# Performance work log

Hardware: AMD Instinct MI355X
Metric: run time of the kernel (lower is better)

## Reference

```python
import jax, jax.numpy as jnp
import numpy as np

T = 3          # hparams['T'] message-passing iterations
E = 100000     # num edges (rows of link_state)
M = 200000     # num message pairs
D = 128        # hidden dim of link_state / GRU units
H = 256        # Message MLP hidden width
G = 64         # num graphs


def setup_inputs() -> dict:
    key = jax.random.key(0)
    ks = jax.random.split(key, 16)
    s = 0.05
    inp = {
        'link_state': jax.random.normal(ks[0], (E, D), jnp.float32),
        'states_first': jax.random.randint(ks[1], (M,), 0, E),
        'states_second': jax.random.randint(ks[2], (M,), 0, E),
        'states_graph_ids': jnp.sort(jax.random.randint(ks[3], (E,), 0, G)),
        'sates_num_edges': E,
        # Message MLP: Dense(H, relu) -> Dense(D, relu)
        'mW1': jax.random.normal(ks[4], (2 * D, H), jnp.float32) * s,
        'mb1': jnp.zeros((H,), jnp.float32),
        'mW2': jax.random.normal(ks[5], (H, D), jnp.float32) * s,
        'mb2': jnp.zeros((D,), jnp.float32),
        # GRUCell (keras, reset_after=True): kernel [D,3D], recurrent [D,3D], bias [2,3D]
        'gru_kernel': jax.random.normal(ks[6], (D, 3 * D), jnp.float32) * s,
        'gru_recurrent': jax.random.normal(ks[7], (D, 3 * D), jnp.float32) * s,
        'gru_bias': jnp.zeros((2, 3 * D), jnp.float32),
        # Readout MLP: Dense(H, relu) -> Dense(H, relu) -> Dense(1)
        'rW1': jax.random.normal(ks[8], (D, H), jnp.float32) * s,
        'rb1': jnp.zeros((H,), jnp.float32),
        'rW2': jax.random.normal(ks[9], (H, H), jnp.float32) * s,
        'rb2': jnp.zeros((H,), jnp.float32),
        'rW3': jax.random.normal(ks[10], (H, 1), jnp.float32) * s,
        'rb3': jnp.zeros((1,), jnp.float32),
    }
    return inp


def _gru_step(x, h, kernel, recurrent, bias):
    # keras GRUCell with reset_after=True; gate order: z, r, h
    mx = x @ kernel + bias[0]          # [N, 3D]
    mh = h @ recurrent + bias[1]       # [N, 3D]
    xz, xr, xh = jnp.split(mx, 3, axis=-1)
    hz, hr, hh = jnp.split(mh, 3, axis=-1)
    z = jax.nn.sigmoid(xz + hz)
    r = jax.nn.sigmoid(xr + hr)
    hcand = jnp.tanh(xh + r * hh)
    return z * h + (1.0 - z) * hcand


def reference(link_state, states_first, states_second, states_graph_ids,
              sates_num_edges, mW1, mb1, mW2, mb2,
              gru_kernel, gru_recurrent, gru_bias,
              rW1, rb1, rW2, rb2, rW3, rb3):
    for _ in range(T):
        main_e = link_state[states_first]        # [M, D] gather
        neigh_e = link_state[states_second]      # [M, D] gather
        concat = jnp.concatenate([main_e, neigh_e], axis=1)  # [M, 2D]
        msg = jax.nn.relu(concat @ mW1 + mb1)
        msg = jax.nn.relu(msg @ mW2 + mb2)       # [M, D]
        edges_inputs = jax.ops.segment_sum(msg, states_second,
                                           num_segments=sates_num_edges)  # [E, D]
        link_state = _gru_step(edges_inputs, link_state,
                               gru_kernel, gru_recurrent, gru_bias)
    graph_state = jax.ops.segment_sum(link_state, states_graph_ids,
                                      num_segments=G)  # [G, D]
    r = jax.nn.relu(graph_state @ rW1 + rb1)
    r = jax.nn.relu(r @ rW2 + rb2)
    return r @ rW3 + rb3  # [G, 1]
```

## Files before the change

### kernel.cpp

```cpp
#include <hip/hip_runtime.h>

#define NUM_E 100000
#define NUM_M 200000
#define DIM   128
#define HID   256
#define NG    64
#define TITER 3
#define NB_SCAN 98
#define GS_ER 128

typedef __attribute__((ext_vector_type(8))) short bf16x8;
typedef __attribute__((ext_vector_type(4))) float f32x4;

__device__ __forceinline__ unsigned short f2bf(float f) {
  unsigned u = __float_as_uint(f);
  u += 0x7FFF + ((u >> 16) & 1);
  return (unsigned short)(u >> 16);
}
__device__ __forceinline__ float bf2f(unsigned short h) {
  return __uint_as_float(((unsigned)h) << 16);
}
__device__ __forceinline__ float sigmoidf_(float v) {
  return 1.f / (1.f + __expf(-v));
}
__device__ __forceinline__ float tanhf_(float u) {
  u = fminf(fmaxf(u, -15.f), 15.f);
  float ex = __expf(-2.f * u);
  return (1.f - ex) / (1.f + ex);
}
__device__ __forceinline__ float relu_(float v) { return fmaxf(v, 0.f); }

#define MFMA(a, b, c) __builtin_amdgcn_mfma_f32_16x16x32_bf16((a), (b), (c), 0, 0, 0)

__global__ void hist_kernel(const int* __restrict__ second, int* __restrict__ counts,
                            float4* __restrict__ gs4) {
  int m = blockIdx.x * blockDim.x + threadIdx.x;
  if (m < NG * DIM / 4) gs4[m] = make_float4(0.f, 0.f, 0.f, 0.f);
  if (m < NUM_M) atomicAdd(&counts[second[m]], 1);
}

__global__ __launch_bounds__(256) void scan1_kernel(const int* __restrict__ counts,
                                                    int* __restrict__ partials) {
  __shared__ int sh[256];
  int b = blockIdx.x, t = threadIdx.x;
  int i0 = b * 1024 + t * 4;
  int c0 = (i0 + 0 < NUM_E) ? counts[i0 + 0] : 0;
  int c1 = (i0 + 1 < NUM_E) ? counts[i0 + 1] : 0;
  int c2 = (i0 + 2 < NUM_E) ? counts[i0 + 2] : 0;
  int c3 = (i0 + 3 < NUM_E) ? counts[i0 + 3] : 0;
  int tsum = c0 + c1 + c2 + c3;
  sh[t] = tsum;
  __syncthreads();
  for (int off = 1; off < 256; off <<= 1) {
    int v = (t >= off) ? sh[t - off] : 0;
    __syncthreads();
    sh[t] += v;
    __syncthreads();
  }
  if (t == 255) partials[b] = sh[255];
}

__global__ void scan2_kernel(const int* __restrict__ partials, int* __restrict__ base,
                             int* __restrict__ rowptr) {
  if (threadIdx.x == 0) {
    int run = 0;
    for (int b = 0; b < NB_SCAN; ++b) { base[b] = run; run += partials[b]; }
    rowptr[NUM_E] = NUM_M;
  }
}

__global__ __launch_bounds__(256) void scan3_kernel(const int* __restrict__ counts,
                                                    const int* __restrict__ base,
                                                    int* __restrict__ rowptr) {
  __shared__ int sh[256];
  int b = blockIdx.x, t = threadIdx.x;
  int i0 = b * 1024 + t * 4;
  int c0 = (i0 + 0 < NUM_E) ? counts[i0 + 0] : 0;
  int c1 = (i0 + 1 < NUM_E) ? counts[i0 + 1] : 0;
  int c2 = (i0 + 2 < NUM_E) ? counts[i0 + 2] : 0;
  int c3 = (i0 + 3 < NUM_E) ? counts[i0 + 3] : 0;
  int tsum = c0 + c1 + c2 + c3;
  sh[t] = tsum;
  __syncthreads();
  for (int off = 1; off < 256; off <<= 1) {
    int v = (t >= off) ? sh[t - off] : 0;
    __syncthreads();
    sh[t] += v;
    __syncthreads();
  }
  int p = base[b] + (sh[t] - tsum);
  if (i0 + 0 < NUM_E) rowptr[i0 + 0] = p;
  if (i0 + 1 < NUM_E) rowptr[i0 + 1] = p + c0;
  if (i0 + 2 < NUM_E) rowptr[i0 + 2] = p + c0 + c1;
  if (i0 + 3 < NUM_E) rowptr[i0 + 3] = p + c0 + c1 + c2;
}

__global__ void scatter_kernel(const int* __restrict__ second,
                               const int* __restrict__ rowptr,
                               int* __restrict__ cursor, int* __restrict__ order) {
  int m = blockIdx.x * blockDim.x + threadIdx.x;
  if (m < NUM_M) {
    int e = second[m];
    int pos = atomicAdd(&cursor[e], 1);
    int idx = rowptr[e] + pos;
    if (idx < rowptr[e + 1]) order[idx] = m;
  }
}

__device__ __forceinline__ void pack_range(
    const float* __restrict__ srcA, const float* __restrict__ srcB, int KrowsA,
    int N, int src_ld, int col_off, unsigned short* __restrict__ dst, int idx) {
  int l = idx & 63;
  int t = idx >> 6;
  int NF = N / 16;
  int nf = t % NF;
  int ks = t / NF;
  int n = nf * 16 + (l & 15) + col_off;
  int k0 = ks * 32 + (l >> 4) * 8;
  unsigned short o[8];
  #pragma unroll
  for (int j = 0; j < 8; ++j) {
    int k = k0 + j;
    const float* src = (k < KrowsA) ? (srcA + (size_t)k * src_ld)
                                    : (srcB + (size_t)(k - KrowsA) * src_ld);
    o[j] = f2bf(src[n]);
  }
  ushort4* d = (ushort4*)(dst + (size_t)idx * 8);
  d[0] = make_ushort4(o[0], o[1], o[2], o[3]);
  d[1] = make_ushort4(o[4], o[5], o[6], o[7]);
}

__global__ __launch_bounds__(256) void prep_kernel(
    const float4* __restrict__ ls4, ushort4* __restrict__ lsb4, int n4,
    const float* __restrict__ mW1, const float* __restrict__ mW2,
    const float* __restrict__ gk,  const float* __restrict__ gr,
    unsigned short* __restrict__ W1p,  unsigned short* __restrict__ W2p,
    unsigned short* __restrict__ Wzrp, unsigned short* __restrict__ Wkhp,
    unsigned short* __restrict__ Wrhp) {
  int i = blockIdx.x * 256 + threadIdx.x;
  if (i < n4) {
    float4 v = ls4[i];
    ushort4 o;
    o.x = f2bf(v.x); o.y = f2bf(v.y); o.z = f2bf(v.z); o.w = f2bf(v.w);
    lsb4[i] = o;
  }
  if      (i < 8192)  pack_range(mW1, mW1, 256, 256, 256, 0,   W1p,  i);
  else if (i < 12288) pack_range(mW2, mW2, 256, 128, 128, 0,   W2p,  i - 8192);
  else if (i < 20480) pack_range(gk,  gr,  128, 256, 384, 0,   Wzrp, i - 12288);
  else if (i < 22528) pack_range(gk,  gk,  128, 128, 384, 256, Wkhp, i - 20480);
  else if (i < 24576) pack_range(gr,  gr,  128, 128, 384, 256, Wrhp, i - 22528);
}

__global__ __launch_bounds__(512, 2) void msg_kernel(
    const unsigned short* __restrict__ lsb,
    const int* __restrict__ first, const int* __restrict__ second,
    const int* __restrict__ order,
    const unsigned short* __restrict__ W1p,
    const float* __restrict__ b1,
    const unsigned short* __restrict__ W2p,
    const float* __restrict__ b2,
    unsigned short* __restrict__ msgout)
{
  constexpr int AST  = 264;
  constexpr int H1ST = 264;
  __shared__ unsigned short actL[2][32 * AST];
  __shared__ unsigned short h1s[2][32 * H1ST];

  const int tid  = threadIdx.x;
  const int wave = tid >> 6;
  const int lane = tid & 63;
  const int c    = lane & 15;
  const int quad = lane >> 4;

  const int sr  = tid >> 5;
  const int shf = (tid >> 4) & 1;
  const int si  = tid & 15;

  const bf16x8* W1f = (const bf16x8*)W1p;
  const bf16x8* W2f = (const bf16x8*)W2p;
  bf16x8 w1r[16];
  #pragma unroll
  for (int ks = 0; ks < 8; ++ks)
    #pragma unroll
    for (int i = 0; i < 2; ++i)
      w1r[ks * 2 + i] = W1f[(ks * 16 + wave * 2 + i) * 64 + lane];
  bf16x8 w2r[8];
  #pragma unroll
  for (int ks = 0; ks < 8; ++ks)
    w2r[ks] = W2f[(ks * 8 + wave) * 64 + lane];

  float4 b1v[2];
  #pragma unroll
  for (int i = 0; i < 2; ++i)
    b1v[i] = *(const float4*)(b1 + (wave * 2 + i) * 16 + quad * 4);
  float4 b2v = *(const float4*)(b2 + wave * 16 + quad * 4);

  const int nTiles = NUM_M / 32;
  const int stride = gridDim.x;
  int tile = blockIdx.x;
  if (tile >= nTiles) return;
  int parity = 0;

  {
    int m1 = order[tile * 32 + sr];
    int m2 = order[tile * 32 + 16 + sr];
    int e1 = shf ? second[m1] : first[m1];
    int e2 = shf ? second[m2] : first[m2];
    bf16x8 v1 = *(const bf16x8*)(lsb + (size_t)e1 * DIM + si * 8);
    bf16x8 v2 = *(const bf16x8*)(lsb + (size_t)e2 * DIM + si * 8);
    *(bf16x8*)&actL[0][sr * AST + shf * 128 + si * 8]        = v1;
    *(bf16x8*)&actL[0][(sr + 16) * AST + shf * 128 + si * 8] = v2;
  }
  int e1n = 0, e2n = 0;
  {
    int t1 = tile + stride;
    if (t1 < nTiles) {
      int m1 = order[t1 * 32 + sr];
      int m2 = order[t1 * 32 + 16 + sr];
      e1n = shf ? second[m1] : first[m1];
      e2n = shf ? second[m2] : first[m2];
    }
  }
  __syncthreads();

  while (true) {
    const int m0 = tile * 32;
    const int next  = tile + stride;
    const int next2 = next + stride;
    const bool have_next  = (next < nTiles);
    const bool have_next2 = (next2 < nTiles);

    bf16x8 sv1, sv2;
    if (have_next) {
      sv1 = *(const bf16x8*)(lsb + (size_t)e1n * DIM + si * 8);
      sv2 = *(const bf16x8*)(lsb + (size_t)e2n * DIM + si * 8);
    }
    int o1 = 0, o2 = 0;
    if (have_next2) {
      o1 = order[next2 * 32 + sr];
      o2 = order[next2 * 32 + 16 + sr];
    }

    const unsigned short* ab = &actL[parity][0];
    f32x4 accA[2], accB[2];
    #pragma unroll
    for (int i = 0; i < 2; ++i) { accA[i] = (f32x4)(0.f); accB[i] = (f32x4)(0.f); }
    #pragma unroll
    for (int ks = 0; ks < 8; ++ks) {
      bf16x8 bA = *(const bf16x8*)&ab[(c)      * AST + ks * 32 + quad * 8];
      bf16x8 bB = *(const bf16x8*)&ab[(16 + c) * AST + ks * 32 + quad * 8];
      #pragma unroll
      for (int i = 0; i < 2; ++i) {
        accA[i] = MFMA(w1r[ks * 2 + i], bA, accA[i]);
        accB[i] = MFMA(w1r[ks * 2 + i], bB, accB[i]);
      }
    }

    if (have_next2) {
      e1n = shf ? second[o1] : first[o1];
      e2n = shf ? second[o2] : first[o2];
    }

    if (have_next) {
      unsigned short* aw = &actL[parity ^ 1][0];
      *(bf16x8*)&aw[sr * AST + shf * 128 + si * 8]        = sv1;
      *(bf16x8*)&aw[(sr + 16) * AST + shf * 128 + si * 8] = sv2;
    }

    unsigned short* hb = &h1s[parity][0];
    #pragma unroll
    for (int i = 0; i < 2; ++i) {
      int n0 = (wave * 2 + i) * 16 + quad * 4;
      ushort4 pa, pb;
      pa.x = f2bf(relu_(accA[i][0] + b1v[i].x));
      pa.y = f2bf(relu_(accA[i][1] + b1v[i].y));
      pa.z = f2bf(relu_(accA[i][2] + b1v[i].z));
      pa.w = f2bf(relu_(accA[i][3] + b1v[i].w));
      pb.x = f2bf(relu_(accB[i][0] + b1v[i].x));
      pb.y = f2bf(relu_(accB[i][1] + b1v[i].y));
      pb.z = f2bf(relu_(accB[i][2] + b1v[i].z));
      pb.w = f2bf(relu_(accB[i][3] + b1v[i].w));
      *(ushort4*)&hb[(c)      * H1ST + n0] = pa;
      *(ushort4*)&hb[(16 + c) * H1ST + n0] = pb;
    }
    __syncthreads();

    f32x4 a2A = (f32x4)(0.f), a2B = (f32x4)(0.f);
    #pragma unroll
    for (int ks2 = 0; ks2 < 8; ++ks2) {
      bf16x8 bA = *(const bf16x8*)&hb[(c)      * H1ST + ks2 * 32 + quad * 8];
      bf16x8 bB = *(const bf16x8*)&hb[(16 + c) * H1ST + ks2 * 32 + quad * 8];
      a2A = MFMA(w2r[ks2], bA, a2A);
      a2B = MFMA(w2r[ks2], bB, a2B);
    }

    {
      int n0 = wave * 16 + quad * 4;
      ushort4 pa, pb;
      pa.x = f2bf(relu_(a2A[0] + b2v.x));
      pa.y = f2bf(relu_(a2A[1] + b2v.y));
      pa.z = f2bf(relu_(a2A[2] + b2v.z));
      pa.w = f2bf(relu_(a2A[3] + b2v.w));
      pb.x = f2bf(relu_(a2B[0] + b2v.x));
      pb.y = f2bf(relu_(a2B[1] + b2v.y));
      pb.z = f2bf(relu_(a2B[2] + b2v.z));
      pb.w = f2bf(relu_(a2B[3] + b2v.w));
      *(ushort4*)(msgout + (size_t)(m0 + c) * DIM + n0)      = pa;
      *(ushort4*)(msgout + (size_t)(m0 + 16 + c) * DIM + n0) = pb;
    }

    if (!have_next) break;
    tile = next;
    parity ^= 1;
  }
}

__device__ __forceinline__ ushort4 gru_gate(
    f32x4 az, f32x4 ar, f32x4 axh, f32x4 ahh, ushort4 hraw,
    float4 bz0, float4 br0, float4 bh0, float4 bz1, float4 br1, float4 bh1) {
  float ho[4] = { bf2f(hraw.x), bf2f(hraw.y), bf2f(hraw.z), bf2f(hraw.w) };
  const float* paz  = (const float*)&az;  const float* par  = (const float*)&ar;
  const float* paxh = (const float*)&axh; const float* pahh = (const float*)&ahh;
  const float* pz0 = (const float*)&bz0; const float* pr0 = (const float*)&br0;
  const float* ph0 = (const float*)&bh0; const float* pz1 = (const float*)&bz1;
  const float* pr1 = (const float*)&br1; const float* ph1 = (const float*)&bh1;
  unsigned short o[4];
  #pragma unroll
  for (int j = 0; j < 4; ++j) {
    float z  = sigmoidf_(paz[j] + pz0[j] + pz1[j]);
    float r  = sigmoidf_(par[j] + pr0[j] + pr1[j]);
    float hc = tanhf_(paxh[j] + ph0[j] + r * (pahh[j] + ph1[j]));
    o[j] = f2bf(z * ho[j] + (1.f - z) * hc);
  }
  return make_ushort4(o[0], o[1], o[2], o[3]);
}

__global__ __launch_bounds__(512, 2) void gru_kernel(
    const unsigned short* __restrict__ msgb,
    const int* __restrict__ rowptr,
    unsigned short* __restrict__ lsb,
    const unsigned short* __restrict__ Wzrp,
    const unsigned short* __restrict__ Wkhp,
    const unsigned short* __restrict__ Wrhp,
    const float* __restrict__ gb)
{
  constexpr int AST = 264;
  __shared__ unsigned short xfL[32 * AST];
  __shared__ unsigned short hfL[32 * AST];

  const int tid  = threadIdx.x;
  const int wave = tid >> 6;
  const int lane = tid & 63;
  const int c    = lane & 15;
  const int quad = lane >> 4;

  const bf16x8* Wzrf = (const bf16x8*)Wzrp;
  const bf16x8* Wkhf = (const bf16x8*)Wkhp;
  const bf16x8* Wrhf = (const bf16x8*)Wrhp;
  bf16x8 wz[8], wr[8];
  #pragma unroll
  for (int ks = 0; ks < 8; ++ks) {
    wz[ks] = Wzrf[(ks * 16 + wave) * 64 + lane];
    wr[ks] = Wzrf[(ks * 16 + 8 + wave) * 64 + lane];
  }
  bf16x8 wxh[4], whh[4];
  #pragma unroll
  for (int ks = 0; ks < 4; ++ks) {
    wxh[ks] = Wkhf[(ks * 8 + wave) * 64 + lane];
    whh[ks] = Wrhf[(ks * 8 + wave) * 64 + lane];
  }

  const float4* gbv = (const float4*)gb;
  const int q4 = wave * 4 + quad;
  const float4 b0z = gbv[q4],      b0r = gbv[32 + q4],  b0h = gbv[64 + q4];
  const float4 b1z = gbv[96 + q4], b1r = gbv[128 + q4], b1h = gbv[160 + q4];

  const int el = wave * 4 + (lane >> 4);
  const int li = lane & 15;

  const int nTiles = NUM_E / 32;
  for (int tile = blockIdx.x; tile < nTiles; tile += gridDim.x) {
    {
      const int e  = tile * 32 + el;
      const int rs = rowptr[e], re = rowptr[e + 1];
      float xs[8];
      #pragma unroll
      for (int j = 0; j < 8; ++j) xs[j] = 0.f;
      for (int p = rs; p < re; ++p) {
        bf16x8 v = *(const bf16x8*)(msgb + (size_t)p * DIM + li * 8);
        #pragma unroll
        for (int j = 0; j < 8; ++j) xs[j] += bf2f((unsigned short)v[j]);
      }
      bf16x8 xv;
      #pragma unroll
      for (int j = 0; j < 8; ++j) xv[j] = (short)f2bf(xs[j]);
      *(bf16x8*)&xfL[el * AST + li * 8] = xv;
      *(bf16x8*)&hfL[el * AST + li * 8] =
          *(const bf16x8*)(lsb + (size_t)e * DIM + li * 8);
    }
    __syncthreads();

    f32x4 zA = (f32x4)(0.f), zB = (f32x4)(0.f);
    f32x4 rA = (f32x4)(0.f), rB = (f32x4)(0.f);
    f32x4 xhA = (f32x4)(0.f), xhB = (f32x4)(0.f);
    f32x4 hhA = (f32x4)(0.f), hhB = (f32x4)(0.f);
    #pragma unroll
    for (int ks = 0; ks < 4; ++ks) {
      bf16x8 xA = *(const bf16x8*)&xfL[(c)      * AST + ks * 32 + quad * 8];
      bf16x8 xB = *(const bf16x8*)&xfL[(16 + c) * AST + ks * 32 + quad * 8];
      bf16x8 hA = *(const bf16x8*)&hfL[(c)      * AST + ks * 32 + quad * 8];
      bf16x8 hB = *(const bf16x8*)&hfL[(16 + c) * AST + ks * 32 + quad * 8];
      zA  = MFMA(wz[ks],     xA, zA);   zB  = MFMA(wz[ks],     xB, zB);
      rA  = MFMA(wr[ks],     xA, rA);   rB  = MFMA(wr[ks],     xB, rB);
      zA  = MFMA(wz[4 + ks], hA, zA);   zB  = MFMA(wz[4 + ks], hB, zB);
      rA  = MFMA(wr[4 + ks], hA, rA);   rB  = MFMA(wr[4 + ks], hB, rB);
      xhA = MFMA(wxh[ks],    xA, xhA);  xhB = MFMA(wxh[ks],    xB, xhB);
      hhA = MFMA(whh[ks],    hA, hhA);  hhB = MFMA(whh[ks],    hB, hhB);
    }

    const int n0 = wave * 16 + quad * 4;
    ushort4 hrawA = *(const ushort4*)&hfL[(c)      * AST + n0];
    ushort4 hrawB = *(const ushort4*)&hfL[(16 + c) * AST + n0];
    ushort4 pkA = gru_gate(zA, rA, xhA, hhA, hrawA, b0z, b0r, b0h, b1z, b1r, b1h);
    ushort4 pkB = gru_gate(zB, rB, xhB, hhB, hrawB, b0z, b0r, b0h, b1z, b1r, b1h);
    *(ushort4*)(lsb + (size_t)(tile * 32 + c) * DIM + n0)      = pkA;
    *(ushort4*)(lsb + (size_t)(tile * 32 + 16 + c) * DIM + n0) = pkB;
    __syncthreads();
  }
}

__global__ __launch_bounds__(256) void graph_sum_kernel(
    const unsigned short* __restrict__ lsb, const int* __restrict__ gids,
    float* __restrict__ gs) {
  const int t = threadIdx.x;
  const int d = t & 127;
  const int half = t >> 7;
  const int e0 = blockIdx.x * GS_ER;
  const int e1 = min(e0 + GS_ER, NUM_E);
  float acc = 0.f;
  int cur = -1;
  for (int e = e0 + half; e < e1; e += 2) {
    int g = gids[e];
    if (g != cur) {
      if (cur >= 0) atomicAdd(&gs[cur * DIM + d], acc);
      acc = 0.f;
      cur = g;
    }
    acc += bf2f(lsb[(size_t)e * DIM + d]);
  }
  if (cur >= 0) atomicAdd(&gs[cur * DIM + d], acc);
}

__global__ __launch_bounds__(256) void readout_kernel(
    const float* __restrict__ gs,
    const float* __restrict__ rW1, const float* __restrict__ rb1,
    const float* __restrict__ rW2, const float* __restrict__ rb2,
    const float* __restrict__ rW3, const float* __restrict__ rb3,
    float* __restrict__ out) {
  __shared__ float shg[DIM];
  __shared__ float sh1[HID];
  __shared__ float red[HID];
  int g = blockIdx.x, c = threadIdx.x;
  if (c < DIM) shg[c] = gs[g * DIM + c];
  __syncthreads();
  float s = rb1[c];
  for (int k = 0; k < DIM; ++k) s += shg[k] * rW1[k * HID + c];
  sh1[c] = relu_(s);
  __syncthreads();
  s = rb2[c];
  for (int k = 0; k < HID; ++k) s += sh1[k] * rW2[k * HID + c];
  red[c] = relu_(s) * rW3[c];
  __syncthreads();
  for (int off = 128; off > 0; off >>= 1) {
    if (c < off) red[c] += red[c + off];
    __syncthreads();
  }
  if (c == 0) out[g] = red[0] + rb3[0];
}

extern "C" void kernel_launch(void* const* d_in, const int* in_sizes, int n_in,
                              void* d_out, int out_size, void* d_ws, size_t ws_size,
                              hipStream_t stream) {
  float* ls          = (float*)d_in[0];
  const int* first   = (const int*)d_in[1];
  const int* second  = (const int*)d_in[2];
  const int* gids    = (const int*)d_in[3];
  const float* mW1   = (const float*)d_in[5];
  const float* mb1   = (const float*)d_in[6];
  const float* mW2   = (const float*)d_in[7];
  const float* mb2   = (const float*)d_in[8];
  const float* gk    = (const float*)d_in[9];
  const float* gr    = (const float*)d_in[10];
  const float* gb    = (const float*)d_in[11];
  const float* rW1   = (const float*)d_in[12];
  const float* rb1   = (const float*)d_in[13];
  const float* rW2   = (const float*)d_in[14];
  const float* rb2   = (const float*)d_in[15];
  const float* rW3   = (const float*)d_in[16];
  const float* rb3   = (const float*)d_in[17];
  float* out = (float*)d_out;

  char* w = (char*)d_ws;
  unsigned short* msgb = (unsigned short*)w;    w += (size_t)NUM_M * DIM * 2;
  unsigned short* lsb  = (unsigned short*)w;    w += (size_t)NUM_E * DIM * 2;
  float* gs    = (float*)w;                     w += NG * DIM * 4;
  int* counts  = (int*)w;                       w += NUM_E * 4;
  int* cursor  = (int*)w;                       w += NUM_E * 4;
  int* rowptr  = (int*)w;                       w += (NUM_E + 4) * 4;
  int* order   = (int*)w;                       w += NUM_M * 4;
  int* partials= (int*)w;                       w += NB_SCAN * 4;
  int* basep   = (int*)w;                       w += NB_SCAN * 4;
  unsigned short* W1p  = (unsigned short*)w;    w += 256 * 256 * 2;
  unsigned short* W2p  = (unsigned short*)w;    w += 256 * 128 * 2;
  unsigned short* Wzrp = (unsigned short*)w;    w += 256 * 256 * 2;
  unsigned short* Wkhp = (unsigned short*)w;    w += 128 * 128 * 2;
  unsigned short* Wrhp = (unsigned short*)w;    w += 128 * 128 * 2;

  const int n4 = NUM_E * DIM / 4;
  prep_kernel<<<(n4 + 255) / 256, 256, 0, stream>>>(
      (const float4*)ls, (ushort4*)lsb, n4, mW1, mW2, gk, gr,
      W1p, W2p, Wzrp, Wkhp, Wrhp);

  hipMemsetAsync(counts, 0, 2 * (size_t)NUM_E * 4, stream);
  hist_kernel<<<(NUM_M + 255) / 256, 256, 0, stream>>>(second, counts, (float4*)gs);
  scan1_kernel<<<NB_SCAN, 256, 0, stream>>>(counts, partials);
  scan2_kernel<<<1, 64, 0, stream>>>(partials, basep, rowptr);
  scan3_kernel<<<NB_SCAN, 256, 0, stream>>>(counts, basep, rowptr);
  scatter_kernel<<<(NUM_M + 255) / 256, 256, 0, stream>>>(second, rowptr, cursor, order);

  for (int t = 0; t < TITER; ++t) {
    msg_kernel<<<512, 512, 0, stream>>>(lsb, first, second, order, W1p, mb1, W2p, mb2, msgb);
    gru_kernel<<<512, 512, 0, stream>>>(msgb, rowptr, lsb, Wzrp, Wkhp, Wrhp, gb);
  }
  graph_sum_kernel<<<(NUM_E + GS_ER - 1) / GS_ER, 256, 0, stream>>>(lsb, gids, gs);
  readout_kernel<<<NG, HID, 0, stream>>>(gs, rW1, rb1, rW2, rb2, rW3, rb3, out);
}
```

Baseline: 602.2 us.

## Double-buffer GRU tiles and prefetch next tile's messages during MFMA

The GRU kernel now keeps two LDS buffers and issues global loads for the next tile's messages (first 8 rows) and hidden rows before running the MFMA gate computation on the current tile, then reduces them afterwards. The segment-sum loop is also unrolled by 8 with clamped addresses, so several loads are in flight at once instead of a serial dependent chain. The grid is halved to 256 blocks, giving each block more tiles to pipeline across. This costs more registers and twice the LDS per block, which may reduce occupancy, and it does extra clamped loads for short segments.

```diff
diff --git a/kernel.cpp b/kernel.cpp
--- a/kernel.cpp
+++ b/kernel.cpp
@@ -29,6 +29,11 @@
   return (1.f - ex) / (1.f + ex);
 }
 __device__ __forceinline__ float relu_(float v) { return fmaxf(v, 0.f); }
+
+__device__ __forceinline__ void acc8(float* xs, bf16x8 v) {
+  #pragma unroll
+  for (int j = 0; j < 8; ++j) xs[j] += bf2f((unsigned short)v[j]);
+}
 
 #define MFMA(a, b, c) __builtin_amdgcn_mfma_f32_16x16x32_bf16((a), (b), (c), 0, 0, 0)
 
@@ -345,8 +350,8 @@
     const float* __restrict__ gb)
 {
   constexpr int AST = 264;
-  __shared__ unsigned short xfL[32 * AST];
-  __shared__ unsigned short hfL[32 * AST];
+  __shared__ unsigned short xfL[2][32 * AST];
+  __shared__ unsigned short hfL[2][32 * AST];
 
   const int tid  = threadIdx.x;
   const int wave = tid >> 6;
@@ -379,37 +384,78 @@
   const int li = lane & 15;
 
   const int nTiles = NUM_E / 32;
-  for (int tile = blockIdx.x; tile < nTiles; tile += gridDim.x) {
-    {
-      const int e  = tile * 32 + el;
-      const int rs = rowptr[e], re = rowptr[e + 1];
-      float xs[8];
+  const int stride = gridDim.x;
+  int tile = blockIdx.x;
+  if (tile >= nTiles) return;
+  int par = 0;
+
+  {
+    const int e  = tile * 32 + el;
+    const int rs = rowptr[e], re = rowptr[e + 1];
+    float xs[8];
+    #pragma unroll
+    for (int j = 0; j < 8; ++j) xs[j] = 0.f;
+    bf16x8 hrow = *(const bf16x8*)(lsb + (size_t)e * DIM + li * 8);
+    for (int p0 = rs; p0 < re; p0 += 8) {
+      const int pm = re - 1;
+      bf16x8 tv[8];
       #pragma unroll
-      for (int j = 0; j < 8; ++j) xs[j] = 0.f;
-      for (int p = rs; p < re; ++p) {
-        bf16x8 v = *(const bf16x8*)(msgb + (size_t)p * DIM + li * 8);
-        #pragma unroll
-        for (int j = 0; j < 8; ++j) xs[j] += bf2f((unsigned short)v[j]);
-      }
-      bf16x8 xv;
+      for (int k = 0; k < 8; ++k)
+        tv[k] = *(const bf16x8*)(msgb + (size_t)min(p0 + k, pm) * DIM + li * 8);
       #pragma unroll
-      for (int j = 0; j < 8; ++j) xv[j] = (short)f2bf(xs[j]);
-      *(bf16x8*)&xfL[el * AST + li * 8] = xv;
-      *(bf16x8*)&hfL[el * AST + li * 8] =
-          *(const bf16x8*)(lsb + (size_t)e * DIM + li * 8);
-    }
-    __syncthreads();
-
+      for (int k = 0; k < 8; ++k)
+        if (p0 + k < re) acc8(xs, tv[k]);
+    }
+    bf16x8 xv;
+    #pragma unroll
+    for (int j = 0; j < 8; ++j) xv[j] = (short)f2bf(xs[j]);
+    *(bf16x8*)&xfL[0][el * AST + li * 8] = xv;
+    *(bf16x8*)&hfL[0][el * AST + li * 8] = hrow;
+  }
+  int rs1 = 0, re1 = 0;
+  if (tile + stride < nTiles) {
+    const int e1 = (tile + stride) * 32 + el;
+    rs1 = rowptr[e1]; re1 = rowptr[e1 + 1];
+  }
+  __syncthreads();
+
+  while (true) {
+    const int nextT = tile + stride;
+    const bool have_next  = (nextT < nTiles);
+    const bool have_next2 = (nextT + stride < nTiles);
+
+    bf16x8 r0, r1, r2, r3, r4, r5, r6, r7, hrow;
+    if (have_next) {
+      const int e1 = nextT * 32 + el;
+      const int pc = min(max(re1 - 1, rs1), NUM_M - 1);
+      r0 = *(const bf16x8*)(msgb + (size_t)min(rs1 + 0, pc) * DIM + li * 8);
+      r1 = *(const bf16x8*)(msgb + (size_t)min(rs1 + 1, pc) * DIM + li * 8);
+      r2 = *(const bf16x8*)(msgb + (size_t)min(rs1 + 2, pc) * DIM + li * 8);
+      r3 = *(const bf16x8*)(msgb + (size_t)min(rs1 + 3, pc) * DIM + li * 8);
+      r4 = *(const bf16x8*)(msgb + (size_t)min(rs1 + 4, pc) * DIM + li * 8);
+      r5 = *(const bf16x8*)(msgb + (size_t)min(rs1 + 5, pc) * DIM + li * 8);
+      r6 = *(const bf16x8*)(msgb + (size_t)min(rs1 + 6, pc) * DIM + li * 8);
+      r7 = *(const bf16x8*)(msgb + (size_t)min(rs1 + 7, pc) * DIM + li * 8);
+      hrow = *(const bf16x8*)(lsb + (size_t)e1 * DIM + li * 8);
+    }
+    int rs2 = 0, re2 = 0;
+    if (have_next2) {
+      const int e2 = (nextT + stride) * 32 + el;
+      rs2 = rowptr[e2]; re2 = rowptr[e2 + 1];
+    }
+
+    const unsigned short* xb = &xfL[par][0];
+    const unsigned short* hb = &hfL[par][0];
     f32x4 zA = (f32x4)(0.f), zB = (f32x4)(0.f);
     f32x4 rA = (f32x4)(0.f), rB = (f32x4)(0.f);
     f32x4 xhA = (f32x4)(0.f), xhB = (f32x4)(0.f);
     f32x4 hhA = (f32x4)(0.f), hhB = (f32x4)(0.f);
     #pragma unroll
     for (int ks = 0; ks < 4; ++ks) {
-      bf16x8 xA = *(const bf16x8*)&xfL[(c)      * AST + ks * 32 + quad * 8];
-      bf16x8 xB = *(const bf16x8*)&xfL[(16 + c) * AST + ks * 32 + quad * 8];
-      bf16x8 hA = *(const bf16x8*)&hfL[(c)      * AST + ks * 32 + quad * 8];
-      bf16x8 hB = *(const bf16x8*)&hfL[(16 + c) * AST + ks * 32 + quad * 8];
+      bf16x8 xA = *(const bf16x8*)&xb[(c)      * AST + ks * 32 + quad * 8];
+      bf16x8 xB = *(const bf16x8*)&xb[(16 + c) * AST + ks * 32 + quad * 8];
+      bf16x8 hA = *(const bf16x8*)&hb[(c)      * AST + ks * 32 + quad * 8];
+      bf16x8 hB = *(const bf16x8*)&hb[(16 + c) * AST + ks * 32 + quad * 8];
       zA  = MFMA(wz[ks],     xA, zA);   zB  = MFMA(wz[ks],     xB, zB);
       rA  = MFMA(wr[ks],     xA, rA);   rB  = MFMA(wr[ks],     xB, rB);
       zA  = MFMA(wz[4 + ks], hA, zA);   zB  = MFMA(wz[4 + ks], hB, zB);
@@ -417,15 +463,50 @@
       xhA = MFMA(wxh[ks],    xA, xhA);  xhB = MFMA(wxh[ks],    xB, xhB);
       hhA = MFMA(whh[ks],    hA, hhA);  hhB = MFMA(whh[ks],    hB, hhB);
     }
-
-    const int n0 = wave * 16 + quad * 4;
-    ushort4 hrawA = *(const ushort4*)&hfL[(c)      * AST + n0];
-    ushort4 hrawB = *(const ushort4*)&hfL[(16 + c) * AST + n0];
-    ushort4 pkA = gru_gate(zA, rA, xhA, hhA, hrawA, b0z, b0r, b0h, b1z, b1r, b1h);
-    ushort4 pkB = gru_gate(zB, rB, xhB, hhB, hrawB, b0z, b0r, b0h, b1z, b1r, b1h);
-    *(ushort4*)(lsb + (size_t)(tile * 32 + c) * DIM + n0)      = pkA;
-    *(ushort4*)(lsb + (size_t)(tile * 32 + 16 + c) * DIM + n0) = pkB;
+    {
+      const int n0 = wave * 16 + quad * 4;
+      ushort4 hrawA = *(const ushort4*)&hb[(c)      * AST + n0];
+      ushort4 hrawB = *(const ushort4*)&hb[(16 + c) * AST + n0];
+      ushort4 pkA = gru_gate(zA, rA, xhA, hhA, hrawA, b0z, b0r, b0h, b1z, b1r, b1h);
+      ushort4 pkB = gru_gate(zB, rB, xhB, hhB, hrawB, b0z, b0r, b0h, b1z, b1r, b1h);
+      *(ushort4*)(lsb + (size_t)(tile * 32 + c) * DIM + n0)      = pkA;
+      *(ushort4*)(lsb + (size_t)(tile * 32 + 16 + c) * DIM + n0) = pkB;
+    }
+
+    if (have_next) {
+      float xs[8];
+      #pragma unroll
+      for (int j = 0; j < 8; ++j) xs[j] = 0.f;
+      if (rs1 + 0 < re1) acc8(xs, r0);
+      if (rs1 + 1 < re1) acc8(xs, r1);
+      if (rs1 + 2 < re1) acc8(xs, r2);
+      if (rs1 + 3 < re1) acc8(xs, r3);
+      if (rs1 + 4 < re1) acc8(xs, r4);
+      if (rs1 + 5 < re1) acc8(xs, r5);
+      if (rs1 + 6 < re1) acc8(xs, r6);
+      if (rs1 + 7 < re1) acc8(xs, r7);
+      for (int p0 = rs1 + 8; p0 < re1; p0 += 8) {
+        const int pm = re1 - 1;
+        bf16x8 tv[8];
+        #pragma unroll
+        for (int k = 0; k < 8; ++k)
+          tv[k] = *(const bf16x8*)(msgb + (size_t)min(p0 + k, pm) * DIM + li * 8);
+        #pragma unroll
+        for (int k = 0; k < 8; ++k)
+          if (p0 + k < re1) acc8(xs, tv[k]);
+      }
+      bf16x8 xv;
+      #pragma unroll
+      for (int j = 0; j < 8; ++j) xv[j] = (short)f2bf(xs[j]);
+      *(bf16x8*)&xfL[par ^ 1][el * AST + li * 8] = xv;
+      *(bf16x8*)&hfL[par ^ 1][el * AST + li * 8] = hrow;
+    }
     __syncthreads();
+    if (!have_next) break;
+    tile = nextT;
+    par ^= 1;
+    rs1 = rs2;
+    re1 = re2;
   }
 }
 
@@ -530,7 +611,7 @@
 
   for (int t = 0; t < TITER; ++t) {
     msg_kernel<<<512, 512, 0, stream>>>(lsb, first, second, order, W1p, mb1, W2p, mb2, msgb);
-    gru_kernel<<<512, 512, 0, stream>>>(msgb, rowptr, lsb, Wzrp, Wkhp, Wrhp, gb);
+    gru_kernel<<<256, 512, 0, stream>>>(msgb, rowptr, lsb, Wzrp, Wkhp, Wrhp, gb);
   }
   graph_sum_kernel<<<(NUM_E + GS_ER - 1) / GS_ER, 256, 0, stream>>>(lsb, gids, gs);
   readout_kernel<<<NG, HID, 0, stream>>>(gs, rW1, rb1, rW2, rb2, rW3, rb3, out);
```

New measurement: 535.6 us. 1.12x faster.
